# Kernel optimization log

Hardware: AMD Instinct MI355X
Metric: run time of the kernel (lower is better)

## Reference

```python
import jax, jax.numpy as jnp
import numpy as np

HEADS = 16
DIM_HEAD = 64
SCALE = DIM_HEAD ** -0.5
EPS = 1e-5


def setup_inputs() -> dict:
    key = jax.random.key(0)
    ks = jax.random.split(key, 4)
    B, S, D = 2, 2048, 1024
    x = jax.random.normal(ks[0], (B, S, D), dtype=jnp.float32)
    gamma = jnp.ones((D,), dtype=jnp.float32)
    beta = jnp.zeros((D,), dtype=jnp.float32)
    w_qkv = jax.random.normal(ks[1], (D, 3 * D), dtype=jnp.float32) * (D ** -0.5)
    w_out = jax.random.normal(ks[2], (D, D), dtype=jnp.float32) * (D ** -0.5)
    b_out = jnp.zeros((D,), dtype=jnp.float32)
    return {"x": x, "gamma": gamma, "beta": beta, "w_qkv": w_qkv,
            "w_out": w_out, "b_out": b_out}


def reference(x, gamma, beta, w_qkv, w_out, b_out):
    B, S, D = x.shape
    # pre-attention LayerNorm (matches triton layernorm kernel math)
    mean = jnp.mean(x, axis=-1, keepdims=True)
    centered = x - mean
    var = jnp.mean(centered * centered, axis=-1, keepdims=True)
    xn = centered * jax.lax.rsqrt(var + EPS) * gamma + beta
    # qkv projection (no bias), split into heads: b s (h d) -> b h s d
    qkv = xn @ w_qkv  # [B, S, 3D]
    q, k, v = jnp.split(qkv, 3, axis=-1)
    split_heads = lambda t: t.reshape(B, S, HEADS, DIM_HEAD).transpose(0, 2, 1, 3)
    q, k, v = split_heads(q) * SCALE, split_heads(k), split_heads(v)
    # unfused attention: full [B,H,S,S] scores, row softmax, then AV
    sim = jnp.einsum('bhid,bhjd->bhij', q, k)
    attn = jax.nn.softmax(sim, axis=-1)
    out = jnp.einsum('bhij,bhjd->bhid', attn, v)
    out = out.transpose(0, 2, 1, 3).reshape(B, S, D)  # merge heads
    return out @ w_out + b_out
```

## Files before the change

kernel.cpp:

```cpp
#include <hip/hip_runtime.h>
#include <hip/hip_bf16.h>

constexpr int Dm = 1024;
constexpr int Sq = 2048;
constexpr int Hh = 16;
constexpr int Dh = 64;
constexpr int Rows = 4096;

typedef __attribute__((ext_vector_type(8))) short bf16x8;
typedef __attribute__((ext_vector_type(8))) _Float16 f16x8;
typedef __attribute__((ext_vector_type(4))) float f32x4;
typedef __attribute__((ext_vector_type(16))) float f32x16;
typedef unsigned short u16;

__device__ inline u16 f2bf(float f) {
  union { float f; unsigned int u; } v; v.f = f;
  unsigned int r = v.u + 0x7FFFu + ((v.u >> 16) & 1u);
  return (u16)(r >> 16);
}
__device__ inline unsigned int pack2(float a, float b) {
  return (unsigned int)f2bf(a) | ((unsigned int)f2bf(b) << 16);
}
__device__ inline u16 f2h(float f) {
  union { _Float16 h; u16 u; } v; v.h = (_Float16)f;
  return v.u;
}
__device__ inline unsigned int pack2h(float a, float b) {
  return (unsigned int)f2h(a) | ((unsigned int)f2h(b) << 16);
}
__device__ inline int pkbf(float lo, float hi) {
  float2 f = {lo, hi};
  __hip_bfloat162 h = __float22bfloat162_rn(f);
  union { __hip_bfloat162 h; int i; } u; u.h = h;
  return u.i;
}
__device__ __forceinline__ void gload16(u16* lds, const u16* g) {
  __builtin_amdgcn_global_load_lds(
      (const __attribute__((address_space(1))) unsigned int*)g,
      (__attribute__((address_space(3))) unsigned int*)lds, 16, 0, 0);
}

template <int BASE>
__device__ inline void mk_frag(const f32x16 s, const int half, int dw[4]) {
  int p0 = pkbf(s[BASE + 0], s[BASE + 1]);
  int p1 = pkbf(s[BASE + 2], s[BASE + 3]);
  int p2 = pkbf(s[BASE + 4], s[BASE + 5]);
  int p3 = pkbf(s[BASE + 6], s[BASE + 7]);
  int t0 = half ? p0 : p2, t1 = half ? p1 : p3;
  int u0 = __shfl_xor(t0, 32), u1 = __shfl_xor(t1, 32);
  dw[0] = half ? u0 : p0;
  dw[1] = half ? u1 : p1;
  dw[2] = half ? p2 : u0;
  dw[3] = half ? p3 : u1;
}

__global__ __launch_bounds__(256) void ln_kernel(
    const float* __restrict__ x, const float* __restrict__ gamma,
    const float* __restrict__ beta, u16* __restrict__ xh) {
  const int row = blockIdx.x;
  const int t = threadIdx.x;
  float4 v = reinterpret_cast<const float4*>(x + (size_t)row * Dm)[t];
  float s = v.x + v.y + v.z + v.w;
  float s2 = v.x * v.x + v.y * v.y + v.z * v.z + v.w * v.w;
#pragma unroll
  for (int off = 32; off > 0; off >>= 1) {
    s += __shfl_down(s, off);
    s2 += __shfl_down(s2, off);
  }
  __shared__ float red[8];
  if ((t & 63) == 0) { red[t >> 6] = s; red[(t >> 6) + 4] = s2; }
  __syncthreads();
  float ts = red[0] + red[1] + red[2] + red[3];
  float ts2 = red[4] + red[5] + red[6] + red[7];
  float mean = ts * (1.0f / Dm);
  float var = ts2 * (1.0f / Dm) - mean * mean;
  float rstd = rsqrtf(var + 1e-5f);
  float4 g = reinterpret_cast<const float4*>(gamma)[t];
  float4 b = reinterpret_cast<const float4*>(beta)[t];
  float o0 = (v.x - mean) * rstd * g.x + b.x;
  float o1 = (v.y - mean) * rstd * g.y + b.y;
  float o2 = (v.z - mean) * rstd * g.z + b.z;
  float o3 = (v.w - mean) * rstd * g.w + b.w;
  uint2 hw = {pack2h(o0, o1), pack2h(o2, o3)};
  *reinterpret_cast<uint2*>(xh + (size_t)row * Dm + t * 4) = hw;
}

__global__ __launch_bounds__(256) void convert_w(
    const float* __restrict__ w, u16* __restrict__ wh, int N) {
  __shared__ float T[64][65];
  const int n0 = blockIdx.x * 64, k0 = blockIdx.y * 64;
  const int t = threadIdx.x;
#pragma unroll
  for (int p = 0; p < 4; ++p) {
    int fid = p * 256 + t;
    int kr = fid >> 4, nn = (fid & 15) * 4;
    float4 v = *reinterpret_cast<const float4*>(w + (size_t)(k0 + kr) * N + n0 + nn);
    T[kr][nn] = v.x; T[kr][nn + 1] = v.y; T[kr][nn + 2] = v.z; T[kr][nn + 3] = v.w;
  }
  __syncthreads();
  const int n = t >> 2, kc = (t & 3) * 16;
  unsigned int hw[8];
#pragma unroll
  for (int i = 0; i < 8; ++i)
    hw[i] = pack2h(T[kc + 2 * i][n], T[kc + 2 * i + 1][n]);
  size_t o = (size_t)(n0 + n) * 1024 + k0 + kc;
  *reinterpret_cast<uint4*>(wh + o) = *reinterpret_cast<uint4*>(&hw[0]);
  *reinterpret_cast<uint4*>(wh + o + 8) = *reinterpret_cast<uint4*>(&hw[4]);
}

template <int BM, int BN, int N, int MODE, int NBN, int NWG, int SPLIT>
__global__ __launch_bounds__(256) void gemm_mfma(
    const u16* __restrict__ Ahg, const u16* __restrict__ Alg,
    const u16* __restrict__ Bhg,
    float* __restrict__ oF, u16* __restrict__ qq, u16* __restrict__ kk,
    u16* __restrict__ vv, const float* __restrict__ bias) {
  constexpr int MF = BM / 32;
  constexpr int NF = BN / 32;
  constexpr int AI = BM / 64;
  constexpr int BI = BN / 64;
  __shared__ __align__(16) u16 Ah[2][BM * 32], Bh[2][BN * 32];
  __shared__ __align__(16) u16 Al[2][SPLIT ? BM * 32 : 8];
  const int tid = threadIdx.x;
  const int wgid = (blockIdx.x & 7) * (NWG / 8) + (blockIdx.x >> 3);
  const int bn = wgid % NBN, bm = wgid / NBN;
  const int wv = tid >> 6, lane = tid & 63;
  const int qn = lane & 15, g = lane >> 4;
  const int wr = wv >> 1, wc = wv & 1;
  const int m0 = bm * BM, n0 = bn * BN;
  const int r4 = lane >> 2, c4 = lane & 3;
  const int c4s = c4 ^ ((r4 >> 1) & 3);
  const int gs = g ^ ((qn >> 1) & 3);

  f32x4 acc[MF][NF];
#pragma unroll
  for (int m = 0; m < MF; ++m)
#pragma unroll
    for (int n = 0; n < NF; ++n) acc[m][n] = (f32x4){0.f, 0.f, 0.f, 0.f};

  auto stage = [&](int bf, int kt2) {
    const int k0 = kt2 * 32;
#pragma unroll
    for (int j = 0; j < AI; ++j) {
      const int sl = wv * AI + j;
      const size_t go = (size_t)(m0 + sl * 16 + r4) * Dm + k0 + c4s * 8;
      gload16(&Ah[bf][sl * 512], Ahg + go);
      if constexpr (SPLIT) gload16(&Al[bf][sl * 512], Alg + go);
    }
#pragma unroll
    for (int j = 0; j < BI; ++j) {
      const int sl = wv * BI + j;
      const size_t go = (size_t)(n0 + sl * 16 + r4) * Dm + k0 + c4s * 8;
      gload16(&Bh[bf][sl * 512], Bhg + go);
    }
  };

  stage(0, 0);
  __syncthreads();
  int buf = 0;

  for (int kt = 0; kt < Dm / 32; ++kt) {
    if (kt + 1 < Dm / 32) stage(buf ^ 1, kt + 1);
    f16x8 af0[MF], af1[MF], bb[NF];
#pragma unroll
    for (int m = 0; m < MF; ++m) {
      const int ro = (wr * (BM / 2) + m * 16 + qn) * 32 + gs * 8;
      af0[m] = *reinterpret_cast<const f16x8*>(&Ah[buf][ro]);
      if constexpr (SPLIT) af1[m] = *reinterpret_cast<const f16x8*>(&Al[buf][ro]);
    }
#pragma unroll
    for (int n = 0; n < NF; ++n) {
      const int ro = (wc * (BN / 2) + n * 16 + qn) * 32 + gs * 8;
      bb[n] = *reinterpret_cast<const f16x8*>(&Bh[buf][ro]);
    }
    __builtin_amdgcn_s_setprio(1);
#pragma unroll
    for (int m = 0; m < MF; ++m)
#pragma unroll
      for (int n = 0; n < NF; ++n) {
        acc[m][n] = __builtin_amdgcn_mfma_f32_16x16x32_f16(af0[m], bb[n], acc[m][n], 0, 0, 0);
        if constexpr (SPLIT)
          acc[m][n] = __builtin_amdgcn_mfma_f32_16x16x32_f16(af1[m], bb[n], acc[m][n], 0, 0, 0);
      }
    __builtin_amdgcn_s_setprio(0);
    __syncthreads();
    buf ^= 1;
  }

  if (MODE == 0) {
    const int which = n0 >> 10;
#pragma unroll
    for (int n = 0; n < NF; ++n) {
      const int c = n0 + wc * (BN / 2) + n * 16 + qn;
      const int d = c & 1023, h = d >> 6, dh = d & 63;
#pragma unroll
      for (int m = 0; m < MF; ++m) {
        const int mr0 = m0 + wr * (BM / 2) + m * 16 + 4 * g;
        const int bb2 = mr0 >> 11, ss = mr0 & 2047;
        if (which == 2) {
          uint2 w = {pack2(acc[m][n][0], acc[m][n][1]),
                     pack2(acc[m][n][2], acc[m][n][3])};
          *reinterpret_cast<uint2*>(&vv[(((size_t)bb2 * Hh + h) * Dh + dh) * Sq + ss]) = w;
        } else {
          u16* dst = (which == 0) ? qq : kk;
          const float sc = (which == 0) ? 0.125f * 1.44269504089f : 1.0f;
#pragma unroll
          for (int r = 0; r < 4; ++r)
            dst[(((size_t)bb2 * Hh + h) * Sq + (ss + r)) * Dh + dh] =
                f2bf(acc[m][n][r] * sc);
        }
      }
    }
  } else {
#pragma unroll
    for (int n = 0; n < NF; ++n) {
      const int c = n0 + wc * (BN / 2) + n * 16 + qn;
      const float bv = bias[c];
#pragma unroll
      for (int m = 0; m < MF; ++m) {
        const int mr0 = m0 + wr * (BM / 2) + m * 16 + 4 * g;
#pragma unroll
        for (int r = 0; r < 4; ++r)
          oF[(size_t)(mr0 + r) * N + c] = acc[m][n][r] + bv;
      }
    }
  }
}

__global__ __launch_bounds__(256, 2) void attn_lds(
    const u16* __restrict__ Q, const u16* __restrict__ K,
    const u16* __restrict__ Vt, u16* __restrict__ Oh) {
  __shared__ __align__(16) u16 Ksh[2][8192];
  __shared__ __align__(16) u16 Vsh[2][8192];
  const int tid = threadIdx.x;
  const int wv = tid >> 6, lane = tid & 63;
  const int ln31 = lane & 31, half = lane >> 5;
  const int n = (blockIdx.x & 7) * 64 + (blockIdx.x >> 3);
  const int bh = n >> 4, qt = n & 15;
  const int q0 = qt * 128 + wv * 32;
  const u16* Qb = Q + ((size_t)bh * Sq + q0) * Dh;
  const u16* Kb = K + (size_t)bh * Sq * Dh;
  const u16* Vb = Vt + (size_t)bh * Dh * Sq;

  auto stage = [&](int bufi, int kt2) {
    if (wv < 2) {
#pragma unroll
      for (int j = 0; j < 8; ++j) {
        const int sl = wv * 8 + j;
        const int r = sl * 8 + (lane >> 3);
        const int c2 = (lane & 7) ^ (r & 7);
        gload16(&Ksh[bufi][sl * 512], Kb + (size_t)(kt2 * 128 + r) * Dh + c2 * 8);
      }
    } else {
#pragma unroll
      for (int j = 0; j < 8; ++j) {
        const int sl = (wv - 2) * 8 + j;
        const int r = sl * 4 + (lane >> 4);
        const int c2 = (lane & 15) ^ (r & 15);
        gload16(&Vsh[bufi][sl * 512], Vb + (size_t)r * Sq + kt2 * 128 + c2 * 8);
      }
    }
  };

  bf16x8 qf[4];
#pragma unroll
  for (int c = 0; c < 4; ++c)
    qf[c] = *reinterpret_cast<const bf16x8*>(Qb + ln31 * Dh + c * 16 + 8 * half);

  union { int4 i; bf16x8 b; } ones;
  ones.i = make_int4(0x3F803F80, 0x3F803F80, 0x3F803F80, 0x3F803F80);

  f32x16 o0, o1, lacc;
#pragma unroll
  for (int j = 0; j < 16; ++j) { o0[j] = 0.f; o1[j] = 0.f; lacc[j] = 0.f; }

  stage(0, 0);
  __syncthreads();
  int buf = 0;

  for (int kt2 = 0; kt2 < 16; ++kt2) {
    if (kt2 + 1 < 16) stage(buf ^ 1, kt2 + 1);
#pragma unroll
    for (int h = 0; h < 2; ++h) {
      bf16x8 kf[2][4];
#pragma unroll
      for (int sub = 0; sub < 2; ++sub)
#pragma unroll
        for (int c = 0; c < 4; ++c) {
          const int row = h * 64 + sub * 32 + ln31;
          kf[sub][c] = *reinterpret_cast<const bf16x8*>(
              &Ksh[buf][row * 64 + (((2 * c + half) ^ (row & 7)) << 3)]);
        }
      f32x16 s0, s1;
#pragma unroll
      for (int j = 0; j < 16; ++j) { s0[j] = 0.f; s1[j] = 0.f; }
      __builtin_amdgcn_s_setprio(1);
#pragma unroll
      for (int c = 0; c < 4; ++c) {
        s0 = __builtin_amdgcn_mfma_f32_32x32x16_bf16(kf[0][c], qf[c], s0, 0, 0, 0);
        s1 = __builtin_amdgcn_mfma_f32_32x32x16_bf16(kf[1][c], qf[c], s1, 0, 0, 0);
      }
      __builtin_amdgcn_s_setprio(0);
      bf16x8 vf[2][4];
#pragma unroll
      for (int h2 = 0; h2 < 2; ++h2)
#pragma unroll
        for (int c = 0; c < 4; ++c) {
          const int row = h2 * 32 + ln31;
          const int ch = (h * 8 + 2 * c + half) ^ (row & 15);
          vf[h2][c] = *reinterpret_cast<const bf16x8*>(
              &Vsh[buf][row * 128 + (ch << 3)]);
        }
#pragma unroll
      for (int j = 0; j < 16; ++j) s0[j] = __builtin_amdgcn_exp2f(s0[j]);
#pragma unroll
      for (int j = 0; j < 16; ++j) s1[j] = __builtin_amdgcn_exp2f(s1[j]);
      int dw[4][4];
      mk_frag<0>(s0, half, dw[0]);
      mk_frag<8>(s0, half, dw[1]);
      mk_frag<0>(s1, half, dw[2]);
      mk_frag<8>(s1, half, dw[3]);
      __builtin_amdgcn_s_setprio(1);
#pragma unroll
      for (int c = 0; c < 4; ++c) {
        union { int4 i; bf16x8 b; } u;
        u.i = make_int4(dw[c][0], dw[c][1], dw[c][2], dw[c][3]);
        o0 = __builtin_amdgcn_mfma_f32_32x32x16_bf16(vf[0][c], u.b, o0, 0, 0, 0);
        o1 = __builtin_amdgcn_mfma_f32_32x32x16_bf16(vf[1][c], u.b, o1, 0, 0, 0);
        lacc = __builtin_amdgcn_mfma_f32_32x32x16_bf16(ones.b, u.b, lacc, 0, 0, 0);
      }
      __builtin_amdgcn_s_setprio(0);
    }
    __syncthreads();
    buf ^= 1;
  }

  const float inv = 1.0f / lacc[0];
  const int b = bh >> 4, hh = bh & 15;
  u16* oph = Oh + ((size_t)(b * Sq) + q0 + ln31) * Dm + hh * 64;
#pragma unroll
  for (int h2 = 0; h2 < 2; ++h2) {
#pragma unroll
    for (int rg = 0; rg < 4; ++rg) {
      const int dh = h2 * 32 + 8 * rg + 4 * half;
      float v0, v1, v2, v3;
      if (h2 == 0) {
        v0 = o0[4 * rg] * inv; v1 = o0[4 * rg + 1] * inv;
        v2 = o0[4 * rg + 2] * inv; v3 = o0[4 * rg + 3] * inv;
      } else {
        v0 = o1[4 * rg] * inv; v1 = o1[4 * rg + 1] * inv;
        v2 = o1[4 * rg + 2] * inv; v3 = o1[4 * rg + 3] * inv;
      }
      uint2 hw = {pack2h(v0, v1), pack2h(v2, v3)};
      *reinterpret_cast<uint2*>(oph + dh) = hw;
    }
  }
}

extern "C" void kernel_launch(void* const* d_in, const int* in_sizes, int n_in,
                              void* d_out, int out_size, void* d_ws, size_t ws_size,
                              hipStream_t stream) {
  const float* x = (const float*)d_in[0];
  const float* gamma = (const float*)d_in[1];
  const float* beta = (const float*)d_in[2];
  const float* w_qkv = (const float*)d_in[3];
  const float* w_out = (const float*)d_in[4];
  const float* b_out = (const float*)d_in[5];
  float* out = (float*)d_out;
  u16* W = (u16*)d_ws;
  const size_t NT = (size_t)Rows * Dm;
  const size_t MT = (size_t)Dm * Dm;
  u16* xh = W;
  u16* Qbf = W + NT;
  u16* Kbf = W + 2 * NT;
  u16* Vbf = W + 3 * NT;
  u16* Ohh = W + 4 * NT;
  u16* wqh = W + 5 * NT;
  u16* woh = wqh + 3 * MT;

  convert_w<<<dim3(48, 16), dim3(256), 0, stream>>>(w_qkv, wqh, 3072);
  convert_w<<<dim3(16, 16), dim3(256), 0, stream>>>(w_out, woh, 1024);
  ln_kernel<<<dim3(Rows), dim3(256), 0, stream>>>(x, gamma, beta, xh);
  gemm_mfma<128, 128, 3072, 0, 24, 768, 0><<<dim3(768), dim3(256), 0, stream>>>(
      xh, nullptr, wqh, nullptr, Qbf, Kbf, Vbf, nullptr);
  attn_lds<<<dim3(512), dim3(256), 0, stream>>>(Qbf, Kbf, Vbf, Ohh);
  gemm_mfma<128, 64, 1024, 1, 16, 512, 0><<<dim3(512), dim3(256), 0, stream>>>(
      Ohh, nullptr, woh, out, nullptr, nullptr, nullptr, b_out);
}
```

Baseline: 130.0 us.

## Split attention KV range across wave pairs and merge partial results in LDS

```diff
diff --git a/kernel.cpp b/kernel.cpp
--- a/kernel.cpp
+++ b/kernel.cpp
@@ -226,37 +226,37 @@
   }
 }
 
-__global__ __launch_bounds__(256, 2) void attn_lds(
+__global__ __launch_bounds__(256, 4) void attn_split2(
     const u16* __restrict__ Q, const u16* __restrict__ K,
     const u16* __restrict__ Vt, u16* __restrict__ Oh) {
-  __shared__ __align__(16) u16 Ksh[2][8192];
-  __shared__ __align__(16) u16 Vsh[2][8192];
+  __shared__ __align__(16) u16 Ksh[2][4096];
+  __shared__ __align__(16) u16 Vsh[2][4096];
   const int tid = threadIdx.x;
   const int wv = tid >> 6, lane = tid & 63;
   const int ln31 = lane & 31, half = lane >> 5;
-  const int n = (blockIdx.x & 7) * 64 + (blockIdx.x >> 3);
-  const int bh = n >> 4, qt = n & 15;
-  const int q0 = qt * 128 + wv * 32;
+  const int qg = wv & 1, kvh = wv >> 1;
+  const int n = (blockIdx.x & 7) * 128 + (blockIdx.x >> 3);
+  const int bh = n >> 5, qt = n & 31;
+  const int q0 = qt * 64 + qg * 32;
   const u16* Qb = Q + ((size_t)bh * Sq + q0) * Dh;
-  const u16* Kb = K + (size_t)bh * Sq * Dh;
-  const u16* Vb = Vt + (size_t)bh * Dh * Sq;
-
-  auto stage = [&](int bufi, int kt2) {
-    if (wv < 2) {
+  const u16* Kb = K + ((size_t)bh * Sq + (size_t)kvh * 1024) * Dh;
+  const u16* Vb = Vt + (size_t)bh * Dh * Sq + kvh * 1024;
+  const int l8 = lane >> 3, c8 = lane & 7;
+
+  auto stage = [&](int t) {
+    if (qg == 0) {
 #pragma unroll
       for (int j = 0; j < 8; ++j) {
-        const int sl = wv * 8 + j;
-        const int r = sl * 8 + (lane >> 3);
-        const int c2 = (lane & 7) ^ (r & 7);
-        gload16(&Ksh[bufi][sl * 512], Kb + (size_t)(kt2 * 128 + r) * Dh + c2 * 8);
+        const int r = j * 8 + l8;
+        const int c2 = c8 ^ (r & 7);
+        gload16(&Ksh[kvh][j * 512], Kb + (size_t)(t * 64 + r) * Dh + c2 * 8);
       }
     } else {
 #pragma unroll
       for (int j = 0; j < 8; ++j) {
-        const int sl = (wv - 2) * 8 + j;
-        const int r = sl * 4 + (lane >> 4);
-        const int c2 = (lane & 15) ^ (r & 15);
-        gload16(&Vsh[bufi][sl * 512], Vb + (size_t)r * Sq + kt2 * 128 + c2 * 8);
+        const int r = j * 8 + l8;
+        const int c2 = c8 ^ (r & 7);
+        gload16(&Vsh[kvh][j * 512], Vb + (size_t)r * Sq + t * 64 + c2 * 8);
       }
     }
   };
@@ -273,85 +273,90 @@
 #pragma unroll
   for (int j = 0; j < 16; ++j) { o0[j] = 0.f; o1[j] = 0.f; lacc[j] = 0.f; }
 
-  stage(0, 0);
+  for (int t = 0; t < 16; ++t) {
+    stage(t);
+    __syncthreads();
+    bf16x8 kf[2][4];
+#pragma unroll
+    for (int sub = 0; sub < 2; ++sub)
+#pragma unroll
+      for (int c = 0; c < 4; ++c) {
+        const int row = sub * 32 + ln31;
+        kf[sub][c] = *reinterpret_cast<const bf16x8*>(
+            &Ksh[kvh][row * 64 + (((2 * c + half) ^ (row & 7)) << 3)]);
+      }
+    f32x16 s0, s1;
+#pragma unroll
+    for (int j = 0; j < 16; ++j) { s0[j] = 0.f; s1[j] = 0.f; }
+    __builtin_amdgcn_s_setprio(1);
+#pragma unroll
+    for (int c = 0; c < 4; ++c) {
+      s0 = __builtin_amdgcn_mfma_f32_32x32x16_bf16(kf[0][c], qf[c], s0, 0, 0, 0);
+      s1 = __builtin_amdgcn_mfma_f32_32x32x16_bf16(kf[1][c], qf[c], s1, 0, 0, 0);
+    }
+    __builtin_amdgcn_s_setprio(0);
+    bf16x8 vf[2][4];
+#pragma unroll
+    for (int h2 = 0; h2 < 2; ++h2)
+#pragma unroll
+      for (int c = 0; c < 4; ++c) {
+        const int row = h2 * 32 + ln31;
+        vf[h2][c] = *reinterpret_cast<const bf16x8*>(
+            &Vsh[kvh][row * 64 + (((2 * c + half) ^ (row & 7)) << 3)]);
+      }
+#pragma unroll
+    for (int j = 0; j < 16; ++j) s0[j] = __builtin_amdgcn_exp2f(s0[j]);
+#pragma unroll
+    for (int j = 0; j < 16; ++j) s1[j] = __builtin_amdgcn_exp2f(s1[j]);
+    int dw[4][4];
+    mk_frag<0>(s0, half, dw[0]);
+    mk_frag<8>(s0, half, dw[1]);
+    mk_frag<0>(s1, half, dw[2]);
+    mk_frag<8>(s1, half, dw[3]);
+    __builtin_amdgcn_s_setprio(1);
+#pragma unroll
+    for (int c = 0; c < 4; ++c) {
+      union { int4 i; bf16x8 b; } u;
+      u.i = make_int4(dw[c][0], dw[c][1], dw[c][2], dw[c][3]);
+      o0 = __builtin_amdgcn_mfma_f32_32x32x16_bf16(vf[0][c], u.b, o0, 0, 0, 0);
+      o1 = __builtin_amdgcn_mfma_f32_32x32x16_bf16(vf[1][c], u.b, o1, 0, 0, 0);
+      lacc = __builtin_amdgcn_mfma_f32_32x32x16_bf16(ones.b, u.b, lacc, 0, 0, 0);
+    }
+    __builtin_amdgcn_s_setprio(0);
+    __syncthreads();
+  }
+
+  float* M = reinterpret_cast<float*>(&Ksh[0][0]);
+  if (kvh == 1) {
+    float* row = M + (qg * 64 + lane) * 33;
+#pragma unroll
+    for (int j = 0; j < 16; ++j) { row[j] = o0[j]; row[16 + j] = o1[j]; }
+    row[32] = lacc[0];
+  }
   __syncthreads();
-  int buf = 0;
-
-  for (int kt2 = 0; kt2 < 16; ++kt2) {
-    if (kt2 + 1 < 16) stage(buf ^ 1, kt2 + 1);
-#pragma unroll
-    for (int h = 0; h < 2; ++h) {
-      bf16x8 kf[2][4];
-#pragma unroll
-      for (int sub = 0; sub < 2; ++sub)
-#pragma unroll
-        for (int c = 0; c < 4; ++c) {
-          const int row = h * 64 + sub * 32 + ln31;
-          kf[sub][c] = *reinterpret_cast<const bf16x8*>(
-              &Ksh[buf][row * 64 + (((2 * c + half) ^ (row & 7)) << 3)]);
+  if (kvh == 0) {
+    const float* row = M + (qg * 64 + lane) * 33;
+#pragma unroll
+    for (int j = 0; j < 16; ++j) { o0[j] += row[j]; o1[j] += row[16 + j]; }
+    const float inv = 1.0f / (lacc[0] + row[32]);
+    const int b = bh >> 4, hh = bh & 15;
+    u16* oph = Oh + ((size_t)(b * Sq) + q0 + ln31) * Dm + hh * 64;
+#pragma unroll
+    for (int h2 = 0; h2 < 2; ++h2) {
+#pragma unroll
+      for (int rg = 0; rg < 4; ++rg) {
+        const int dh = h2 * 32 + 8 * rg + 4 * half;
+        float v0, v1, v2, v3;
+        if (h2 == 0) {
+          v0 = o0[4 * rg] * inv; v1 = o0[4 * rg + 1] * inv;
+          v2 = o0[4 * rg + 2] * inv; v3 = o0[4 * rg + 3] * inv;
+        } else {
+          v0 = o1[4 * rg] * inv; v1 = o1[4 * rg + 1] * inv;
+          v2 = o1[4 * rg + 2] * inv; v3 = o1[4 * rg + 3] * inv;
         }
-      f32x16 s0, s1;
-#pragma unroll
-      for (int j = 0; j < 16; ++j) { s0[j] = 0.f; s1[j] = 0.f; }
-      __builtin_amdgcn_s_setprio(1);
-#pragma unroll
-      for (int c = 0; c < 4; ++c) {
-        s0 = __builtin_amdgcn_mfma_f32_32x32x16_bf16(kf[0][c], qf[c], s0, 0, 0, 0);
-        s1 = __builtin_amdgcn_mfma_f32_32x32x16_bf16(kf[1][c], qf[c], s1, 0, 0, 0);
-      }
-      __builtin_amdgcn_s_setprio(0);
-      bf16x8 vf[2][4];
-#pragma unroll
-      for (int h2 = 0; h2 < 2; ++h2)
-#pragma unroll
-        for (int c = 0; c < 4; ++c) {
-          const int row = h2 * 32 + ln31;
-          const int ch = (h * 8 + 2 * c + half) ^ (row & 15);
-          vf[h2][c] = *reinterpret_cast<const bf16x8*>(
-              &Vsh[buf][row * 128 + (ch << 3)]);
-        }
-#pragma unroll
-      for (int j = 0; j < 16; ++j) s0[j] = __builtin_amdgcn_exp2f(s0[j]);
-#pragma unroll
-      for (int j = 0; j < 16; ++j) s1[j] = __builtin_amdgcn_exp2f(s1[j]);
-      int dw[4][4];
-      mk_frag<0>(s0, half, dw[0]);
-      mk_frag<8>(s0, half, dw[1]);
-      mk_frag<0>(s1, half, dw[2]);
-      mk_frag<8>(s1, half, dw[3]);
-      __builtin_amdgcn_s_setprio(1);
-#pragma unroll
-      for (int c = 0; c < 4; ++c) {
-        union { int4 i; bf16x8 b; } u;
-        u.i = make_int4(dw[c][0], dw[c][1], dw[c][2], dw[c][3]);
-        o0 = __builtin_amdgcn_mfma_f32_32x32x16_bf16(vf[0][c], u.b, o0, 0, 0, 0);
-        o1 = __builtin_amdgcn_mfma_f32_32x32x16_bf16(vf[1][c], u.b, o1, 0, 0, 0);
-        lacc = __builtin_amdgcn_mfma_f32_32x32x16_bf16(ones.b, u.b, lacc, 0, 0, 0);
-      }
-      __builtin_amdgcn_s_setprio(0);
-    }
-    __syncthreads();
-    buf ^= 1;
-  }
-
-  const float inv = 1.0f / lacc[0];
-  const int b = bh >> 4, hh = bh & 15;
-  u16* oph = Oh + ((size_t)(b * Sq) + q0 + ln31) * Dm + hh * 64;
-#pragma unroll
-  for (int h2 = 0; h2 < 2; ++h2) {
-#pragma unroll
-    for (int rg = 0; rg < 4; ++rg) {
-      const int dh = h2 * 32 + 8 * rg + 4 * half;
-      float v0, v1, v2, v3;
-      if (h2 == 0) {
-        v0 = o0[4 * rg] * inv; v1 = o0[4 * rg + 1] * inv;
-        v2 = o0[4 * rg + 2] * inv; v3 = o0[4 * rg + 3] * inv;
-      } else {
-        v0 = o1[4 * rg] * inv; v1 = o1[4 * rg + 1] * inv;
-        v2 = o1[4 * rg + 2] * inv; v3 = o1[4 * rg + 3] * inv;
-      }
-      uint2 hw = {pack2h(v0, v1), pack2h(v2, v3)};
-      *reinterpret_cast<uint2*>(oph + dh) = hw;
+        uint2 hw = {pack2h(v0, v1), pack2h(v2, v3)};
+        *reinterpret_cast<uint2*>(oph + dh) = hw;
+      }
     }
   }
 }
@@ -382,7 +387,7 @@
   ln_kernel<<<dim3(Rows), dim3(256), 0, stream>>>(x, gamma, beta, xh);
   gemm_mfma<128, 128, 3072, 0, 24, 768, 0><<<dim3(768), dim3(256), 0, stream>>>(
       xh, nullptr, wqh, nullptr, Qbf, Kbf, Vbf, nullptr);
-  attn_lds<<<dim3(512), dim3(256), 0, stream>>>(Qbf, Kbf, Vbf, Ohh);
+  attn_split2<<<dim3(1024), dim3(256), 0, stream>>>(Qbf, Kbf, Vbf, Ohh);
   gemm_mfma<128, 64, 1024, 1, 16, 512, 0><<<dim3(512), dim3(256), 0, stream>>>(
       Ohh, nullptr, woh, out, nullptr, nullptr, nullptr, b_out);
 }
```

Result: slower. 252.5 us (+94.2%).
